# Performance work log

Hardware: AMD Instinct MI355X
Metric: run time of the kernel (lower is better)

Reference implementation:

```python
import jax, jax.numpy as jnp
import numpy as np

T = 4096      # tokens (flattened batch*seq)
DIN = 2048    # input hidden dim
DQ = 2048     # q output dim
DKV = 2048    # per-head-group kv output dim (== DQ here, MHA)
NA = 4        # number of adapters (LoRA/delta models)
R = 16        # lora rank per q/k/v


def setup_inputs() -> dict:
    key = jax.random.key(0)
    ks = jax.random.split(key, 8)
    def rn(k, shape, scale):
        return jax.random.normal(k, shape, dtype=jnp.float32) * scale
    return {
        "x": rn(ks[0], (T, DIN), 1.0),
        "W_base": rn(ks[1], (DQ + 2 * DKV, DIN), DIN ** -0.5),
        "A_buffer_qkv": rn(ks[2], (NA, DIN, 3 * R), DIN ** -0.5),
        "B_buffer_q": rn(ks[3], (NA, R, DQ), R ** -0.5),
        "B_buffer_kv": rn(ks[4], (NA, R, 2 * DKV), R ** -0.5),
        "DeltaW_q": rn(ks[5], (NA, DIN, DQ), DIN ** -0.5),
        "DeltaW_kv": rn(ks[6], (NA, DIN, 2 * DKV), DIN ** -0.5),
        "weight_indices": jax.random.randint(ks[7], (T,), 0, NA, dtype=jnp.int32),
    }


def _ldmm(indices, x, A, B, D):
    """Per-token adapter-indexed (LoRA + dense delta) matmul.
    indices: [T] int, x: [T, din], A: [na, din, r], B: [na, r, dout], D: [na, din, dout].
    out[t] = (x[t] @ A[a]) @ B[a] + x[t] @ D[a]  with a = indices[t].
    Implemented as masked GEMMs over the small fixed adapter set.
    """
    na = A.shape[0]
    out = jnp.zeros((x.shape[0], B.shape[2]), dtype=x.dtype)
    for a in range(na):  # small fixed loop over adapters
        xa = jnp.where((indices == a)[:, None], x, jnp.zeros((), x.dtype))
        out = out + (xa @ A[a]) @ B[a] + xa @ D[a]
    return out


def reference(x, W_base, A_buffer_qkv, B_buffer_q, B_buffer_kv,
              DeltaW_q, DeltaW_kv, weight_indices):
    # base QKV projection (ColumnParallelLinear, no bias): [T, dq + 2*dkv]
    base = x @ W_base.T
    rank = A_buffer_qkv.shape[2] // 3
    b_dim_q = B_buffer_q.shape[2]
    b_dim_kv = B_buffer_kv.shape[2] // 2
    d_dim_kv = DeltaW_kv.shape[2] // 2
    for i in range(3):  # q, k, v slices
        if i == 0:
            o = _ldmm(weight_indices, x,
                      A_buffer_qkv[:, :, :rank], B_buffer_q, DeltaW_q)
            base = base.at[:, :b_dim_q].add(o)
        else:
            o = _ldmm(weight_indices, x,
                      A_buffer_qkv[:, :, i * rank:(i + 1) * rank],
                      B_buffer_kv[:, :, (i - 1) * b_dim_kv:i * b_dim_kv],
                      DeltaW_kv[:, :, (i - 1) * d_dim_kv:i * d_dim_kv])
            base = base.at[:, i * b_dim_kv:(i + 1) * b_dim_kv].add(o)
    return base
```

## Files before the change

### kernel.cpp

```cpp
#include <hip/hip_runtime.h>
#include <stdint.h>

#define T_TOK 4096
#define DIN   2048
#define DQ    2048
#define DKV   2048
#define NOUT  (DQ + 2*DKV)
#define NA    4
#define RLORA 16
#define BM    256
#define BN    256
#define MPAD  (T_TOK + NA*BM)
#define MTILES (MPAD/BM)
#define KX    (DIN + 64)
#define NKT   (KX/32)
#define KSPLIT 16
#define NTBLK (NOUT/BN)
#define NWG   (MTILES*NTBLK)

typedef unsigned short u16;
typedef __attribute__((ext_vector_type(8))) short short8;
typedef __attribute__((ext_vector_type(8))) u16 u16x8;
typedef __attribute__((ext_vector_type(4))) float f32x4;

__device__ __forceinline__ u16 f2bf(float f) {
  uint32_t u = __float_as_uint(f);
  u = (u + 0x7FFFu + ((u >> 16) & 1u)) >> 16;
  return (u16)u;
}
__device__ __forceinline__ float bf2f(u16 u) {
  return __uint_as_float(((uint32_t)u) << 16);
}

typedef __attribute__((address_space(3))) void lds_void;
typedef __attribute__((address_space(1))) void glb_void;

__device__ __forceinline__ void gl_lds16(const void* g, void* l) {
  __builtin_amdgcn_global_load_lds((const glb_void*)(uintptr_t)g,
                                   (lds_void*)(uint32_t)(uintptr_t)l, 16, 0, 0);
}

__global__ void prep_kernel(const int* __restrict__ widx,
                            int* __restrict__ tok,
                            int* __restrict__ tileAdapter) {
  __shared__ int cnt[256][NA];
  __shared__ int total[NA];
  __shared__ int pad_off[NA];
  const int tid = threadIdx.x;
  const int CH = T_TOK / 256;
  const int base = tid * CH;
  int c[NA] = {0, 0, 0, 0};
  for (int i = 0; i < CH; i++) c[widx[base + i]]++;
  for (int a = 0; a < NA; a++) cnt[tid][a] = c[a];
  __syncthreads();
  if (tid < NA) {
    int s = 0;
    for (int i = 0; i < 256; i++) { int v = cnt[i][tid]; cnt[i][tid] = s; s += v; }
    total[tid] = s;
  }
  __syncthreads();
  if (tid == 0) {
    int off = 0;
    for (int a = 0; a < NA; a++) {
      pad_off[a] = off;
      int ntile = (total[a] + BM - 1) / BM;
      for (int tl = 0; tl < ntile; tl++) tileAdapter[off / BM + tl] = a;
      off += ntile * BM;
    }
    for (int tl = off / BM; tl < MTILES; tl++) tileAdapter[tl] = -1;
  }
  __syncthreads();
  for (int i = tid; i < MPAD; i += 256) tok[i] = -1;
  __syncthreads();
  int myoff[NA];
  for (int a = 0; a < NA; a++) myoff[a] = pad_off[a] + cnt[tid][a];
  for (int i = 0; i < CH; i++) {
    int a = widx[base + i];
    tok[myoff[a]++] = base + i;
  }
}

__global__ void gather_kernel(const float* __restrict__ x,
                              const int* __restrict__ tok,
                              u16* __restrict__ Xg) {
  const int row = blockIdx.x;
  const int t = tok[row];
  const int tid = threadIdx.x;
  u16x8* dst = (u16x8*)(Xg + (size_t)row * KX);
  if (t < 0) {
    u16x8 z = {0, 0, 0, 0, 0, 0, 0, 0};
    dst[tid] = z;
    return;
  }
  const f32x4* src = (const f32x4*)(x + (size_t)t * DIN);
  f32x4 v0 = src[tid * 2];
  f32x4 v1 = src[tid * 2 + 1];
  u16x8 o;
  o[0] = f2bf(v0[0]); o[1] = f2bf(v0[1]); o[2] = f2bf(v0[2]); o[3] = f2bf(v0[3]);
  o[4] = f2bf(v1[0]); o[5] = f2bf(v1[1]); o[6] = f2bf(v1[2]); o[7] = f2bf(v1[3]);
  dst[tid] = o;
}

__global__ __launch_bounds__(256) void xa_partial_kernel(
    const u16* __restrict__ Xg, const float* __restrict__ A_qkv,
    const int* __restrict__ tileAdapter, float* __restrict__ Ppart) {
  const int ks = blockIdx.y;
  const int ad = tileAdapter[blockIdx.x >> 1];
  const int a = ad < 0 ? 0 : ad;
  const int kb = ks * (DIN / KSPLIT);
  const int tid = threadIdx.x;
  const int rg = tid >> 2;
  const int jg = tid & 3;
  const int r0 = blockIdx.x * 128 + rg * 2;
  const int j0 = jg * 12;
  __shared__ float ldsA[64][56];
  float acc[2][12];
  #pragma unroll
  for (int r = 0; r < 2; r++)
    #pragma unroll
    for (int j = 0; j < 12; j++) acc[r][j] = 0.f;

  for (int kc = 0; kc < 2; kc++) {
    const int kbase = kb + kc * 64;
    for (int i = tid; i < 64 * 48; i += 256) {
      int kk = i / 48, j = i - kk * 48;
      ldsA[kk][j] = A_qkv[((size_t)a * DIN + kbase + kk) * (3 * RLORA) + j];
    }
    __syncthreads();
    u16x8 xr[2][8];
    #pragma unroll
    for (int r = 0; r < 2; r++)
      #pragma unroll
      for (int q = 0; q < 8; q++)
        xr[r][q] = *(const u16x8*)(Xg + (size_t)(r0 + r) * KX + kbase + q * 8);
    #pragma unroll
    for (int q = 0; q < 8; q++) {
      #pragma unroll
      for (int e = 0; e < 8; e++) {
        const int kk = q * 8 + e;
        f32x4 a0 = *(const f32x4*)&ldsA[kk][j0];
        f32x4 a1 = *(const f32x4*)&ldsA[kk][j0 + 4];
        f32x4 a2 = *(const f32x4*)&ldsA[kk][j0 + 8];
        float x0 = bf2f(xr[0][q][e]);
        float x1 = bf2f(xr[1][q][e]);
        #pragma unroll
        for (int c = 0; c < 4; c++) {
          acc[0][c]     += x0 * a0[c];  acc[1][c]     += x1 * a0[c];
          acc[0][4 + c] += x0 * a1[c];  acc[1][4 + c] += x1 * a1[c];
          acc[0][8 + c] += x0 * a2[c];  acc[1][8 + c] += x1 * a2[c];
        }
      }
    }
    __syncthreads();
  }
  #pragma unroll
  for (int r = 0; r < 2; r++)
    #pragma unroll
    for (int j = 0; j < 12; j++)
      Ppart[((size_t)ks * MPAD + r0 + r) * 48 + j0 + j] = acc[r][j];
}

__global__ void xa_reduce_kernel(const float* __restrict__ Ppart,
                                 u16* __restrict__ Xg) {
  const int gid = blockIdx.x * 256 + threadIdx.x;
  const int row = gid >> 6, j = gid & 63;
  float s = 0.f;
  if (j < 48) {
    #pragma unroll
    for (int sp = 0; sp < KSPLIT; sp++)
      s += Ppart[((size_t)sp * MPAD + row) * 48 + j];
  }
  Xg[(size_t)row * KX + DIN + j] = f2bf(s);
}

__global__ __launch_bounds__(256) void weff2_kernel(
    const float* __restrict__ W_base,
    const float* __restrict__ DW_q, const float* __restrict__ DW_kv,
    u16* __restrict__ Weff) {
  const int k0 = blockIdx.x * 64;
  const int n0 = blockIdx.y * 64;
  const int tid = threadIdx.x;
  const int k8 = (tid & 7) * 8;
  __shared__ float ldsD[64][65];

  f32x4 wb[2][2];
  #pragma unroll
  for (int h = 0; h < 2; h++) {
    const int nn = h * 32 + (tid >> 3);
    const float* p = W_base + (size_t)(n0 + nn) * DIN + k0 + k8;
    wb[h][0] = *(const f32x4*)p;
    wb[h][1] = *(const f32x4*)(p + 4);
  }

  const int ldD  = (n0 < DQ) ? DQ : 2 * DKV;
  const int ncol = (n0 < DQ) ? n0 : n0 - DQ;

  for (int a = 0; a < NA; a++) {
    const float* Dp = (n0 < DQ)
        ? DW_q  + (size_t)a * DIN * DQ + ncol
        : DW_kv + (size_t)a * DIN * (2 * DKV) + ncol;
    for (int i = tid; i < 64 * 64; i += 256) {
      int kk = i >> 6, nn2 = i & 63;
      ldsD[kk][nn2] = Dp[(size_t)(k0 + kk) * ldD + nn2];
    }
    __syncthreads();
    #pragma unroll
    for (int h = 0; h < 2; h++) {
      const int nn = h * 32 + (tid >> 3);
      u16x8 o;
      #pragma unroll
      for (int j = 0; j < 8; j++)
        o[j] = f2bf(wb[h][j >> 2][j & 3] + ldsD[k8 + j][nn]);
      *(u16x8*)(Weff + ((size_t)a * NOUT + n0 + nn) * KX + k0 + k8) = o;
    }
    __syncthreads();
  }
}

__global__ void wslots_kernel(const float* __restrict__ B_q,
                              const float* __restrict__ B_kv,
                              u16* __restrict__ Weff) {
  const int a = blockIdx.y;
  const int n = blockIdx.x * 256 + threadIdx.x;
  const int seg = n >> 11;
  u16 vals[64];
  #pragma unroll
  for (int j = 0; j < 64; j++) vals[j] = 0;
  if (seg == 0) {
    const float* Bp = B_q + ((size_t)a * RLORA) * DQ + n;
    #pragma unroll
    for (int r = 0; r < RLORA; r++) vals[r] = f2bf(Bp[(size_t)r * DQ]);
  } else if (seg == 1) {
    const float* Bp = B_kv + ((size_t)a * RLORA) * (2 * DKV) + (n - DQ);
    #pragma unroll
    for (int r = 0; r < RLORA; r++) vals[RLORA + r] = f2bf(Bp[(size_t)r * (2 * DKV)]);
  } else {
    const float* Bp = B_kv + ((size_t)a * RLORA) * (2 * DKV) + (n - DQ);
    #pragma unroll
    for (int r = 0; r < RLORA; r++) vals[2 * RLORA + r] = f2bf(Bp[(size_t)r * (2 * DKV)]);
  }
  u16* dst = Weff + ((size_t)a * NOUT + n) * KX + DIN;
  #pragma unroll
  for (int v = 0; v < 8; v++) *(u16x8*)(dst + v * 8) = *(u16x8*)(vals + v * 8);
}

#define BAR      asm volatile("s_barrier" ::: "memory")
#define WAITV(n) asm volatile("s_waitcnt vmcnt(" #n ")" ::: "memory")

#define STAGE(b, t) { \
  const u16* gA_ = gAs + (size_t)(t) * 32; \
  const u16* gB_ = gBs + (size_t)(t) * 32; \
  u16* lA_ = &lds[b][0][0] + tid * 8; \
  u16* lB_ = &lds[b][1][0] + tid * 8; \
  gl_lds16(gA_, lA_); \
  gl_lds16(gA_ + (size_t)128 * KX, lA_ + 4096); \
  gl_lds16(gB_, lB_); \
  gl_lds16(gB_ + (size_t)128 * KX, lB_ + 4096); \
}

#define COMPUTE(b) { \
  const char* Ab = (const char*)&lds[b][0][0]; \
  const char* Bb = (const char*)&lds[b][1][0]; \
  short8 af[8], bfr[4]; \
  _Pragma("unroll") for (int mi = 0; mi < 8; ++mi) \
    af[mi] = *(const short8*)(Ab + (wm * 128 + mi * 16) * 64 + laneoff); \
  _Pragma("unroll") for (int ni = 0; ni < 4; ++ni) \
    bfr[ni] = *(const short8*)(Bb + (wn * 64 + ni * 16) * 64 + laneoff); \
  __builtin_amdgcn_s_setprio(1); \
  _Pragma("unroll") for (int mi = 0; mi < 8; ++mi) \
  _Pragma("unroll") for (int ni = 0; ni < 4; ++ni) \
    acc[mi][ni] = __builtin_amdgcn_mfma_f32_16x16x32_bf16( \
        af[mi], bfr[ni], acc[mi][ni], 0, 0, 0); \
  __builtin_amdgcn_s_setprio(0); \
}

__global__ __launch_bounds__(512, 2) void gemm256_kernel(
    const u16* __restrict__ Xg, const u16* __restrict__ Weff,
    const int* __restrict__ tok, const int* __restrict__ tileAdapter,
    float* __restrict__ out) {
  __shared__ __align__(16) u16 lds[4][2][256 * 32];

  const int bid = blockIdx.x;
  const int wg = (bid & 7) * (NWG / 8) + (bid >> 3);
  const int mt = wg % MTILES, nt = wg / MTILES;
  const int a = tileAdapter[mt];
  if (a < 0) return;
  const int m0 = mt * BM, n0 = nt * BN;

  const int tid = threadIdx.x;
  const int l = tid & 63, w = tid >> 6;
  const int wm = w >> 2, wn = w & 3;
  const int fr = l & 15;
  const int laneoff = fr * 64 + ((((l >> 4) ^ ((fr >> 1) & 3))) << 4);

  const int srow = tid >> 2;
  const int scol = (((tid & 3) ^ ((tid >> 3) & 3))) * 8;
  const u16* gAs = Xg + (size_t)(m0 + srow) * KX + scol;
  const u16* gBs = Weff + ((size_t)a * NOUT + n0 + srow) * KX + scol;

  f32x4 acc[8][4];
  #pragma unroll
  for (int i = 0; i < 8; i++)
    #pragma unroll
    for (int j = 0; j < 4; j++) acc[i][j] = (f32x4){0.f, 0.f, 0.f, 0.f};

  STAGE(0, 0);
  STAGE(1, 1);
  STAGE(2, 2);

  for (int i = 0; i < NKT - 3; ++i) {
    WAITV(8);
    BAR;
    STAGE((i + 3) & 3, i + 3);
    COMPUTE(i & 3);
  }
  WAITV(8); BAR; COMPUTE((NKT - 3) & 3);
  WAITV(4); BAR; COMPUTE((NKT - 2) & 3);
  WAITV(0); BAR; COMPUTE((NKT - 1) & 3);

  #pragma unroll
  for (int mi = 0; mi < 8; ++mi) {
    const int rb = m0 + wm * 128 + mi * 16 + ((l >> 4) << 2);
    int tt[4];
    #pragma unroll
    for (int reg = 0; reg < 4; ++reg) tt[reg] = tok[rb + reg];
    #pragma unroll
    for (int ni = 0; ni < 4; ++ni) {
      const int col = n0 + wn * 64 + ni * 16 + fr;
      #pragma unroll
      for (int reg = 0; reg < 4; ++reg)
        if (tt[reg] >= 0) out[(size_t)tt[reg] * NOUT + col] = acc[mi][ni][reg];
    }
  }
}

__global__ void fallback_kernel(const float* __restrict__ x,
                                const float* __restrict__ W_base,
                                const float* __restrict__ A_qkv,
                                const float* __restrict__ B_q,
                                const float* __restrict__ B_kv,
                                const float* __restrict__ DW_q,
                                const float* __restrict__ DW_kv,
                                const int* __restrict__ widx,
                                float* __restrict__ out) {
  const int t = blockIdx.x;
  const int n = blockIdx.y * 256 + threadIdx.x;
  const int a = widx[t];
  __shared__ float xs[DIN];
  __shared__ float ys[3 * RLORA];
  for (int k = threadIdx.x; k < DIN; k += 256) xs[k] = x[(size_t)t * DIN + k];
  __syncthreads();
  if (threadIdx.x < 3 * RLORA) {
    float s = 0.f;
    const float* Ap = A_qkv + (size_t)a * DIN * (3 * RLORA) + threadIdx.x;
    for (int k = 0; k < DIN; k++) s += xs[k] * Ap[(size_t)k * (3 * RLORA)];
    ys[threadIdx.x] = s;
  }
  __syncthreads();
  const float* dcol; int ldD, roff; const float* bcol; int ldB;
  if (n < DQ) {
    dcol = DW_q + (size_t)a * DIN * DQ + n; ldD = DQ; roff = 0;
    bcol = B_q + (size_t)a * RLORA * DQ + n; ldB = DQ;
  } else {
    dcol = DW_kv + (size_t)a * DIN * (2 * DKV) + (n - DQ); ldD = 2 * DKV;
    roff = (n < 2 * DQ) ? RLORA : 2 * RLORA;
    bcol = B_kv + (size_t)a * RLORA * (2 * DKV) + (n - DQ); ldB = 2 * DKV;
  }
  const float* wrow = W_base + (size_t)n * DIN;
  float acc = 0.f;
  for (int k = 0; k < DIN; k++) acc += xs[k] * (wrow[k] + dcol[(size_t)k * ldD]);
  for (int r = 0; r < RLORA; r++) acc += ys[roff + r] * bcol[(size_t)r * ldB];
  out[(size_t)t * NOUT + n] = acc;
}

extern "C" void kernel_launch(void* const* d_in, const int* in_sizes, int n_in,
                              void* d_out, int out_size, void* d_ws, size_t ws_size,
                              hipStream_t stream) {
  const float* x      = (const float*)d_in[0];
  const float* W_base = (const float*)d_in[1];
  const float* A_qkv  = (const float*)d_in[2];
  const float* B_q    = (const float*)d_in[3];
  const float* B_kv   = (const float*)d_in[4];
  const float* DW_q   = (const float*)d_in[5];
  const float* DW_kv  = (const float*)d_in[6];
  const int*   widx   = (const int*)d_in[7];
  float* out = (float*)d_out;

  const size_t WEFF_BYTES = (size_t)NA * NOUT * KX * sizeof(u16);
  const size_t XG_BYTES   = (size_t)MPAD * KX * sizeof(u16);
  const size_t TOK_BYTES  = (size_t)MPAD * sizeof(int);
  const size_t TILE_BYTES = (size_t)MTILES * sizeof(int);
  const size_t need = WEFF_BYTES + XG_BYTES + TOK_BYTES + TILE_BYTES;

  if (ws_size < need) {
    fallback_kernel<<<dim3(T_TOK, NOUT / 256), 256, 0, stream>>>(
        x, W_base, A_qkv, B_q, B_kv, DW_q, DW_kv, widx, out);
    return;
  }

  char* ws = (char*)d_ws;
  u16* Weff = (u16*)ws;
  u16* Xg   = (u16*)(ws + WEFF_BYTES);
  int* tok  = (int*)(ws + WEFF_BYTES + XG_BYTES);
  int* tileAdapter = tok + MPAD;
  float* Ppart = (float*)ws;

  prep_kernel<<<1, 256, 0, stream>>>(widx, tok, tileAdapter);
  gather_kernel<<<MPAD, 256, 0, stream>>>(x, tok, Xg);
  xa_partial_kernel<<<dim3(MPAD / 128, KSPLIT), 256, 0, stream>>>(
      Xg, A_qkv, tileAdapter, Ppart);
  xa_reduce_kernel<<<MPAD * 64 / 256, 256, 0, stream>>>(Ppart, Xg);
  weff2_kernel<<<dim3(DIN / 64, NOUT / 64), 256, 0, stream>>>(
      W_base, DW_q, DW_kv, Weff);
  wslots_kernel<<<dim3(NOUT / 256, NA), 256, 0, stream>>>(B_q, B_kv, Weff);
  gemm256_kernel<<<dim3(NWG), 512, 0, stream>>>(
      Xg, Weff, tok, tileAdapter, out);
}
```

Measured before the change: 262.8 us.

## Restructure GEMM mainloop to K=64 tiles with quadrant-interleaved loads

The main GEMM loop now uses K=64 steps with a double-buffered LDS layout instead of a 4-stage K=32 ring. Each K tile is split into four quadrant sub-steps (A and B halves). Each sub-step interleaves LDS fragment reads, global-to-LDS prefetches for the next tiles, and MFMA bursts, separated by barriers. An 8-way XOR swizzle is used to avoid bank conflicts. The aim is finer-grained overlap of memory and compute at fewer pipeline stages, at the cost of many more barriers and a hand-scheduled, fragile prologue and epilogue.

```diff
diff --git a/kernel.cpp b/kernel.cpp
--- a/kernel.cpp
+++ b/kernel.cpp
@@ -13,7 +13,7 @@
 #define MPAD  (T_TOK + NA*BM)
 #define MTILES (MPAD/BM)
 #define KX    (DIN + 64)
-#define NKT   (KX/32)
+#define NKT64 (KX/64)
 #define KSPLIT 16
 #define NTBLK (NOUT/BN)
 #define NWG   (MTILES*NTBLK)
@@ -247,38 +247,63 @@
 #define BAR      asm volatile("s_barrier" ::: "memory")
 #define WAITV(n) asm volatile("s_waitcnt vmcnt(" #n ")" ::: "memory")
 
-#define STAGE(b, t) { \
-  const u16* gA_ = gAs + (size_t)(t) * 32; \
-  const u16* gB_ = gBs + (size_t)(t) * 32; \
-  u16* lA_ = &lds[b][0][0] + tid * 8; \
-  u16* lB_ = &lds[b][1][0] + tid * 8; \
-  gl_lds16(gA_, lA_); \
-  gl_lds16(gA_ + (size_t)128 * KX, lA_ + 4096); \
-  gl_lds16(gB_, lB_); \
-  gl_lds16(gB_ + (size_t)128 * KX, lB_ + 4096); \
-}
-
-#define COMPUTE(b) { \
-  const char* Ab = (const char*)&lds[b][0][0]; \
-  const char* Bb = (const char*)&lds[b][1][0]; \
-  short8 af[8], bfr[4]; \
-  _Pragma("unroll") for (int mi = 0; mi < 8; ++mi) \
-    af[mi] = *(const short8*)(Ab + (wm * 128 + mi * 16) * 64 + laneoff); \
-  _Pragma("unroll") for (int ni = 0; ni < 4; ++ni) \
-    bfr[ni] = *(const short8*)(Bb + (wn * 64 + ni * 16) * 64 + laneoff); \
+#define RD_A(db, mh) { \
+  _Pragma("unroll") for (int q = 0; q < 4; ++q) { \
+    const char* rp = ldsc + (db)*32768 + (wm*128 + (mh)*64 + q*16 + fr)*128; \
+    af[q][0] = *(const short8*)(rp + ck0); \
+    af[q][1] = *(const short8*)(rp + ck1); } }
+
+#define RD_B(db, nh, bfv) { \
+  _Pragma("unroll") for (int q = 0; q < 2; ++q) { \
+    const char* rp = ldsc + 65536 + (db)*32768 + ((nh)*128 + wn*32 + q*16 + fr)*128; \
+    bfv[q][0] = *(const short8*)(rp + ck0); \
+    bfv[q][1] = *(const short8*)(rp + ck1); } }
+
+#define ST_A(db, mh, t) { \
+  gl_lds16(gAsrc + (size_t)((mh)*64)*KX + (size_t)(t)*64, \
+           ldsu + (db)*16384 + ((mh)*64*64) + stid); \
+  gl_lds16(gAsrc + (size_t)(128 + (mh)*64)*KX + (size_t)(t)*64, \
+           ldsu + (db)*16384 + ((128 + (mh)*64)*64) + stid); }
+
+#define ST_B(db, nh, t) { \
+  gl_lds16(gBsrc + (size_t)((nh)*32)*KX + (size_t)(t)*64, \
+           ldsu + 32768 + (db)*16384 + ((nh)*128*64) + stid); \
+  gl_lds16(gBsrc + (size_t)(128 + (nh)*32)*KX + (size_t)(t)*64, \
+           ldsu + 32768 + (db)*16384 + (((nh)*128 + 64)*64) + stid); }
+
+#define MM(mh, nh, bfv) { \
   __builtin_amdgcn_s_setprio(1); \
-  _Pragma("unroll") for (int mi = 0; mi < 8; ++mi) \
-  _Pragma("unroll") for (int ni = 0; ni < 4; ++ni) \
-    acc[mi][ni] = __builtin_amdgcn_mfma_f32_16x16x32_bf16( \
-        af[mi], bfr[ni], acc[mi][ni], 0, 0, 0); \
-  __builtin_amdgcn_s_setprio(0); \
-}
+  _Pragma("unroll") for (int q = 0; q < 4; ++q) \
+  _Pragma("unroll") for (int r = 0; r < 2; ++r) { \
+    acc[(mh)*4+q][(nh)*2+r] = __builtin_amdgcn_mfma_f32_16x16x32_bf16( \
+        af[q][0], bfv[r][0], acc[(mh)*4+q][(nh)*2+r], 0, 0, 0); \
+    acc[(mh)*4+q][(nh)*2+r] = __builtin_amdgcn_mfma_f32_16x16x32_bf16( \
+        af[q][1], bfv[r][1], acc[(mh)*4+q][(nh)*2+r], 0, 0, 0); } \
+  __builtin_amdgcn_s_setprio(0); }
+
+#define KT_STD(db, t) { \
+  RD_A(db, 0); RD_B(db, 0, bf0); ST_A(1-(db), 1, (t)+1); BAR; MM(0, 0, bf0); BAR; \
+  RD_B(db, 1, bf1);              ST_B(1-(db), 0, (t)+1); BAR; MM(0, 1, bf1); BAR; \
+  RD_A(db, 1);                   ST_A(db, 0, (t)+2);     BAR; MM(1, 1, bf1); BAR; \
+  ST_B(db, 1, (t)+2); WAITV(4);                          BAR; MM(1, 0, bf0); BAR; }
+
+#define KT_T31(db, t) { \
+  RD_A(db, 0); RD_B(db, 0, bf0); ST_A(1-(db), 1, (t)+1); BAR; MM(0, 0, bf0); BAR; \
+  RD_B(db, 1, bf1);              ST_B(1-(db), 0, (t)+1); BAR; MM(0, 1, bf1); BAR; \
+  RD_A(db, 1);                                           BAR; MM(1, 1, bf1); BAR; \
+  WAITV(0);                                              BAR; MM(1, 0, bf0); BAR; }
+
+#define KT_LAST(db) { \
+  RD_A(db, 0); RD_B(db, 0, bf0); BAR; MM(0, 0, bf0); BAR; \
+  RD_B(db, 1, bf1);              BAR; MM(0, 1, bf1); BAR; \
+  RD_A(db, 1);                   BAR; MM(1, 1, bf1); BAR; \
+                                 BAR; MM(1, 0, bf0); BAR; }
 
 __global__ __launch_bounds__(512, 2) void gemm256_kernel(
     const u16* __restrict__ Xg, const u16* __restrict__ Weff,
     const int* __restrict__ tok, const int* __restrict__ tileAdapter,
     float* __restrict__ out) {
-  __shared__ __align__(16) u16 lds[4][2][256 * 32];
+  __shared__ __align__(16) u16 Lds[65536];
 
   const int bid = blockIdx.x;
   const int wg = (bid & 7) * (NWG / 8) + (bid >> 3);
@@ -291,12 +316,20 @@
   const int l = tid & 63, w = tid >> 6;
   const int wm = w >> 2, wn = w & 3;
   const int fr = l & 15;
-  const int laneoff = fr * 64 + ((((l >> 4) ^ ((fr >> 1) & 3))) << 4);
-
-  const int srow = tid >> 2;
-  const int scol = (((tid & 3) ^ ((tid >> 3) & 3))) * 8;
-  const u16* gAs = Xg + (size_t)(m0 + srow) * KX + scol;
-  const u16* gBs = Weff + ((size_t)a * NOUT + n0 + srow) * KX + scol;
+  const int kq = l >> 4;
+  const int s7 = l & 7;
+  const int ck0 = ((kq ^ s7) << 4);
+  const int ck1 = (((4 + kq) ^ s7) << 4);
+
+  const int l64 = tid >> 3;
+  const int swc = (tid & 7) ^ (l64 & 7);
+  const int stid = tid * 8;
+  const u16* gAsrc = Xg + (size_t)(m0 + l64) * KX + swc * 8;
+  const int nB = ((l64 >> 5) * 64) + (l64 & 31);
+  const u16* gBsrc = Weff + ((size_t)a * NOUT + n0 + nB) * KX + swc * 8;
+
+  u16* ldsu = &Lds[0];
+  const char* ldsc = (const char*)ldsu;
 
   f32x4 acc[8][4];
   #pragma unroll
@@ -304,19 +337,21 @@
     #pragma unroll
     for (int j = 0; j < 4; j++) acc[i][j] = (f32x4){0.f, 0.f, 0.f, 0.f};
 
-  STAGE(0, 0);
-  STAGE(1, 1);
-  STAGE(2, 2);
-
-  for (int i = 0; i < NKT - 3; ++i) {
-    WAITV(8);
-    BAR;
-    STAGE((i + 3) & 3, i + 3);
-    COMPUTE(i & 3);
-  }
-  WAITV(8); BAR; COMPUTE((NKT - 3) & 3);
-  WAITV(4); BAR; COMPUTE((NKT - 2) & 3);
-  WAITV(0); BAR; COMPUTE((NKT - 1) & 3);
+  short8 af[4][2], bf0[2][2], bf1[2][2];
+
+  ST_A(0, 0, 0); ST_B(0, 0, 0); ST_A(0, 1, 0); ST_B(0, 1, 0);
+  ST_A(1, 0, 1); ST_B(1, 1, 1);
+  WAITV(4);
+  BAR;
+
+  for (int p = 0; p < 15; ++p) {
+    const int t0 = 2 * p;
+    KT_STD(0, t0);
+    KT_STD(1, t0 + 1);
+  }
+  KT_STD(0, 30);
+  KT_T31(1, 31);
+  KT_LAST(0);
 
   #pragma unroll
   for (int mi = 0; mi < 8; ++mi) {
```

After: 248.5 us. -5.4%, faster.
